# Performance work log

Measured on AMD Instinct MI355X. Metric: run time of the kernel, lower is better.

The kernel has to match this reference:

```python
import jax, jax.numpy as jnp
import numpy as np

N = 200000          # total nodes across the batch of graphs
IN_DIM = 320        # pooling_dim (256) + num_context_attrs (64)
POOL_DIM = 256      # output_dim
HID = 128
NUM_GRAPHS = 2000


def setup_inputs() -> dict:
    key = jax.random.key(0)
    k = jax.random.split(key, 6)
    z = jax.random.normal(k[0], (N, IN_DIM), dtype=jnp.float32)
    batch_index = jnp.sort(jax.random.randint(k[1], (N,), 0, NUM_GRAPHS, dtype=jnp.int64))
    # Kaiming-ish small init to keep softmax well-conditioned
    W1 = jax.random.normal(k[2], (HID, IN_DIM), dtype=jnp.float32) * (1.0 / np.sqrt(IN_DIM))
    b1 = jax.random.normal(k[3], (HID,), dtype=jnp.float32) * 0.01
    W2 = jax.random.normal(k[4], (1, HID), dtype=jnp.float32) * (1.0 / np.sqrt(HID))
    b2 = jax.random.normal(k[5], (1,), dtype=jnp.float32) * 0.01
    return {"z": z, "batch_index": batch_index, "W1": W1, "b1": b1,
            "W2": W2, "b2": b2, "num_graphs": NUM_GRAPHS}


def reference(z, batch_index, W1, b1, W2, b2, num_graphs):
    # attention_net: Linear -> ReLU -> Linear, scores: [N, 1]
    h = jax.nn.relu(z @ W1.T + b1)                  # [N, HID]
    scores = h @ W2.T + b2                          # [N, 1]
    # global (over all nodes) max-subtract + softmax along dim 0
    scores = scores - jnp.max(scores, axis=0, keepdims=True)
    weights = jax.nn.softmax(scores, axis=0)        # [N, 1]
    # weighted scatter-mean over graphs keyed by batch_index
    weighted = weights * z[:, :POOL_DIM]            # [N, POOL_DIM]
    sums = jax.ops.segment_sum(weighted, batch_index, num_segments=num_graphs)  # [G, POOL_DIM]
    counts = jax.ops.segment_sum(jnp.ones((z.shape[0],), dtype=z.dtype),
                                 batch_index, num_segments=num_graphs)          # [G]
    pooled = sums / jnp.maximum(counts, 1.0)[:, None]
    return pooled
```

## Files before the change

### kernel.cpp

```cpp
#include <hip/hip_runtime.h>

#define IN_DIM   320
#define POOL_DIM 256
#define HID      128
#define RPB      128
#define NKC      10

typedef __attribute__((ext_vector_type(8))) short bf16x8;
typedef __attribute__((ext_vector_type(4))) float f32x4;

typedef __attribute__((address_space(1))) const unsigned int guint;
typedef __attribute__((address_space(3))) unsigned int luint;

__device__ __forceinline__ void gl_lds16(const void* g, void* l) {
    __builtin_amdgcn_global_load_lds((guint*)g, (luint*)l, 16, 0, 0);
}

__device__ __forceinline__ unsigned fbits(float f) {
    union { float f; unsigned u; } c; c.f = f; return c.u;
}
__device__ __forceinline__ unsigned pack2(unsigned u0, unsigned u1) {
    return __builtin_amdgcn_perm(u1, u0, 0x07060302u);
}

__device__ __forceinline__ void split8(float4 a, float4 b, bf16x8& hi, bf16x8& lo) {
    float f[8] = { a.x, a.y, a.z, a.w, b.x, b.y, b.z, b.w };
    unsigned hu[8], lu[8];
#pragma unroll
    for (int i = 0; i < 8; ++i) {
        unsigned u = fbits(f[i]);
        hu[i] = u;
        float hif = __builtin_bit_cast(float, u & 0xffff0000u);
        lu[i] = fbits(f[i] - hif);
    }
    int4 hp, lp;
    hp.x = pack2(hu[0], hu[1]); hp.y = pack2(hu[2], hu[3]);
    hp.z = pack2(hu[4], hu[5]); hp.w = pack2(hu[6], hu[7]);
    lp.x = pack2(lu[0], lu[1]); lp.y = pack2(lu[2], lu[3]);
    lp.z = pack2(lu[4], lu[5]); lp.w = pack2(lu[6], lu[7]);
    hi = __builtin_bit_cast(bf16x8, hp);
    lo = __builtin_bit_cast(bf16x8, lp);
}

__global__ __launch_bounds__(256) void pack_w1_kernel(
    const float* __restrict__ W1, ushort* __restrict__ Wpk)
{
    const int i = blockIdx.x * 256 + threadIdx.x;
    if (i >= NKC * 8 * 2 * 64) return;
    const int kc   = i >> 10;
    const int r    = i & 1023;
    const int ht   = r >> 7;
    const int r2   = r & 127;
    const int s    = r2 >> 6;
    const int lane = r2 & 63;
    const int h    = ht * 16 + (lane & 15);
    const int k0   = kc * 32 + (lane >> 4) * 8;

    ushort v[8];
#pragma unroll
    for (int j = 0; j < 8; ++j) {
        const float f = W1[(size_t)h * IN_DIM + k0 + j];
        const unsigned u = fbits(f);
        if (s == 0) {
            v[j] = (ushort)(u >> 16);
        } else {
            const float hif = __builtin_bit_cast(float, u & 0xffff0000u);
            v[j] = (ushort)(fbits(f - hif) >> 16);
        }
    }
    ushort* dst = Wpk + (size_t)i * 8;
#pragma unroll
    for (int j = 0; j < 8; ++j) dst[j] = v[j];
}

__global__ __launch_bounds__(256) void attn_scores_mfma(
    const float* __restrict__ z, const ushort* __restrict__ Wpk,
    const float* __restrict__ b1, const float* __restrict__ W2,
    const float* __restrict__ b2,
    float* __restrict__ scores, float* __restrict__ bmax,
    float* __restrict__ bsum, int N)
{
    __shared__ float4 wbuf[2][1024];
    __shared__ float4 zbuf[2][1024];
    __shared__ float  sblk[RPB];

    const int tid  = threadIdx.x;
    const int wid  = tid >> 6;
    const int lane = tid & 63;
    const int lm   = lane & 15;
    const int lg   = lane >> 4;
    const int r0   = blockIdx.x * RPB;

    const char* zsrc[4];
#pragma unroll
    for (int j = 0; j < 4; ++j) {
        const int s   = tid + j * 256;
        const int row = s >> 3;
        const int q   = (s & 7) ^ (row & 7);
        int gr = r0 + row; if (gr > N - 1) gr = N - 1;
        zsrc[j] = (const char*)z + (size_t)gr * (IN_DIM * 4) + q * 16;
    }

    #define STAGE_W(kc_, b_)                                                  \
        { const char* src = (const char*)Wpk + (size_t)(kc_) * 16384;         \
          char* dst = (char*)&wbuf[b_][0];                                    \
          _Pragma("unroll")                                                   \
          for (int j = 0; j < 4; ++j) {                                       \
              const int o = (tid + j * 256) * 16;                             \
              gl_lds16(src + o, dst + o);                                     \
          } }

    #define STAGE_Z(kc_, b_)                                                  \
        { char* dst = (char*)&zbuf[b_][0];                                    \
          _Pragma("unroll")                                                   \
          for (int j = 0; j < 4; ++j) {                                       \
              const int o = (tid + j * 256) * 16;                             \
              gl_lds16(zsrc[j] + (kc_) * 128, dst + o);                       \
          } }

    f32x4 acc[2][8];
#pragma unroll
    for (int rt = 0; rt < 2; ++rt)
#pragma unroll
        for (int ht = 0; ht < 8; ++ht) acc[rt][ht] = (f32x4){0.f, 0.f, 0.f, 0.f};

    const int lr0 = wid * 32 + lm;
    const int lr1 = lr0 + 16;
    const int i00 = lr0 * 8 + ((2 * lg)     ^ (lr0 & 7));
    const int i01 = lr0 * 8 + ((2 * lg + 1) ^ (lr0 & 7));
    const int i10 = lr1 * 8 + ((2 * lg)     ^ (lr1 & 7));
    const int i11 = lr1 * 8 + ((2 * lg + 1) ^ (lr1 & 7));

    STAGE_Z(0, 0);
    STAGE_W(0, 0);
    __syncthreads();

#pragma unroll
    for (int kc = 0; kc < NKC; ++kc) {
        const int cb  = kc & 1;
        const int nb2 = cb ^ 1;

        if (kc + 1 < NKC) {
            STAGE_Z(kc + 1, nb2);
            STAGE_W(kc + 1, nb2);
        }

        bf16x8 a0h, a0l, a1h, a1l;
        {
            const float4* zb = &zbuf[cb][0];
            const float4 x0 = zb[i00];
            const float4 x1 = zb[i01];
            const float4 y0 = zb[i10];
            const float4 y1 = zb[i11];
            split8(x0, x1, a0h, a0l);
            split8(y0, y1, a1h, a1l);
        }

        const char* wb_base = (const char*)&wbuf[cb][0] + lane * 16;
#pragma unroll
        for (int ht = 0; ht < 8; ++ht) {
            const bf16x8 bh = *(const bf16x8*)(wb_base + ht * 2048);
            const bf16x8 bl = *(const bf16x8*)(wb_base + ht * 2048 + 1024);
            acc[0][ht] = __builtin_amdgcn_mfma_f32_16x16x32_bf16(a0h, bh, acc[0][ht], 0, 0, 0);
            acc[0][ht] = __builtin_amdgcn_mfma_f32_16x16x32_bf16(a0l, bh, acc[0][ht], 0, 0, 0);
            acc[0][ht] = __builtin_amdgcn_mfma_f32_16x16x32_bf16(a0h, bl, acc[0][ht], 0, 0, 0);
            acc[1][ht] = __builtin_amdgcn_mfma_f32_16x16x32_bf16(a1h, bh, acc[1][ht], 0, 0, 0);
            acc[1][ht] = __builtin_amdgcn_mfma_f32_16x16x32_bf16(a1l, bh, acc[1][ht], 0, 0, 0);
            acc[1][ht] = __builtin_amdgcn_mfma_f32_16x16x32_bf16(a1h, bl, acc[1][ht], 0, 0, 0);
        }

        if (kc + 1 < NKC) __syncthreads();
    }

    float b1v[8], w2v[8];
#pragma unroll
    for (int ht = 0; ht < 8; ++ht) {
        b1v[ht] = b1[ht * 16 + lm];
        w2v[ht] = W2[ht * 16 + lm];
    }
    const float b2v = b2[0];

#pragma unroll
    for (int rt = 0; rt < 2; ++rt) {
#pragma unroll
        for (int reg = 0; reg < 4; ++reg) {
            float s = 0.f;
#pragma unroll
            for (int ht = 0; ht < 8; ++ht)
                s += fmaxf(acc[rt][ht][reg] + b1v[ht], 0.f) * w2v[ht];
            s += __shfl_xor(s, 1);
            s += __shfl_xor(s, 2);
            s += __shfl_xor(s, 4);
            s += __shfl_xor(s, 8);
            s += b2v;
            if (lm == 0) {
                const int rloc = wid * 32 + rt * 16 + lg * 4 + reg;
                const int grow = r0 + rloc;
                if (grow < N) {
                    scores[grow] = s;
                    sblk[rloc] = s;
                } else {
                    sblk[rloc] = -1e30f;
                }
            }
        }
    }
    __syncthreads();

    if (tid < 64) {
        const float v0 = sblk[tid];
        const float v1 = sblk[tid + 64];
        float m = fmaxf(v0, v1);
#pragma unroll
        for (int d = 1; d < 64; d <<= 1) m = fmaxf(m, __shfl_xor(m, d, 64));
        float e = __expf(v0 - m) + __expf(v1 - m);
#pragma unroll
        for (int d = 1; d < 64; d <<= 1) e += __shfl_xor(e, d, 64);
        if (tid == 0) {
            bmax[blockIdx.x] = m;
            bsum[blockIdx.x] = e;
        }
    }
}

__global__ __launch_bounds__(256) void softmax_reduce_kernel(
    const float* __restrict__ bmax, const float* __restrict__ bsum,
    float* __restrict__ red, int nb)
{
    __shared__ float sm[4];
    __shared__ float ss[4];
    const int tid = threadIdx.x;

    float m = -1e30f;
    for (int i = tid; i < nb; i += 256) m = fmaxf(m, bmax[i]);
#pragma unroll
    for (int d = 1; d < 64; d <<= 1) m = fmaxf(m, __shfl_xor(m, d, 64));
    if ((tid & 63) == 0) sm[tid >> 6] = m;
    __syncthreads();
    const float gmax = fmaxf(fmaxf(sm[0], sm[1]), fmaxf(sm[2], sm[3]));

    float s = 0.f;
    for (int i = tid; i < nb; i += 256) s += bsum[i] * __expf(bmax[i] - gmax);
#pragma unroll
    for (int d = 1; d < 64; d <<= 1) s += __shfl_xor(s, d, 64);
    if ((tid & 63) == 0) ss[tid >> 6] = s;
    __syncthreads();
    if (tid == 0) {
        red[0] = gmax;
        red[1] = ss[0] + ss[1] + ss[2] + ss[3];
    }
}

__device__ __forceinline__ int lower_bound(const int* __restrict__ a, int n, int key)
{
    int lo = 0, hi = n;
    while (lo < hi) {
        int mid = (lo + hi) >> 1;
        if (a[mid] < key) lo = mid + 1; else hi = mid;
    }
    return lo;
}

__global__ __launch_bounds__(256) void pool_kernel(
    const float* __restrict__ z, const int* __restrict__ bidx,
    const float* __restrict__ scores, const float* __restrict__ red,
    float* __restrict__ out, int N)
{
    const int g    = blockIdx.x;
    const int lane = threadIdx.x & 63;
    const int rg   = threadIdx.x >> 6;
    __shared__ int se[2];
    __shared__ f32x4 pred[4][64];

    if (threadIdx.x == 0) {
        se[0] = lower_bound(bidx, N, g);
        se[1] = lower_bound(bidx, N, g + 1);
    }
    __syncthreads();
    const int start = se[0], end = se[1];
    const float gmax    = red[0];
    const float inv_den = 1.0f / red[1];

    const f32x4* zf = (const f32x4*)z;

    f32x4 acc = (f32x4){0.f, 0.f, 0.f, 0.f};
    for (int i = start + rg; i < end; i += 4) {
        const float w = __expf(scores[i] - gmax);
        acc += w * zf[(size_t)i * 80 + lane];
    }
    pred[rg][lane] = acc;
    __syncthreads();

    if (rg == 0) {
        const f32x4 s = (pred[0][lane] + pred[1][lane]) +
                        (pred[2][lane] + pred[3][lane]);
        const int cnt = end - start;
        const float sc = inv_den / fmaxf((float)cnt, 1.0f);
        ((f32x4*)out)[(size_t)g * 64 + lane] = s * sc;
    }
}

extern "C" void kernel_launch(void* const* d_in, const int* in_sizes, int n_in,
                              void* d_out, int out_size, void* d_ws, size_t ws_size,
                              hipStream_t stream)
{
    const float* z    = (const float*)d_in[0];
    const int*   bidx = (const int*)  d_in[1];
    const float* W1   = (const float*)d_in[2];
    const float* b1   = (const float*)d_in[3];
    const float* W2   = (const float*)d_in[4];
    const float* b2   = (const float*)d_in[5];
    float*       out  = (float*)d_out;

    const int N  = in_sizes[0] / IN_DIM;
    const int G  = out_size / POOL_DIM;
    const int nb = (N + RPB - 1) / RPB;

    float*  scores = (float*)d_ws;
    float*  bmax   = scores + 200000;
    float*  bsum   = bmax + 1600;
    float*  red    = bsum + 1600;
    ushort* Wpk    = (ushort*)(red + 16);

    pack_w1_kernel<<<(NKC * 8 * 2 * 64 + 255) / 256, 256, 0, stream>>>(W1, Wpk);
    attn_scores_mfma<<<nb, 256, 0, stream>>>(z, Wpk, b1, W2, b2,
                                             scores, bmax, bsum, N);
    softmax_reduce_kernel<<<1, 256, 0, stream>>>(bmax, bsum, red, nb);
    pool_kernel<<<G, 256, 0, stream>>>(z, bidx, scores, red, out, N);
}
```

Measured before the change: 116.8 us.

## Fuse segment pooling into score kernel by keeping z tile resident in LDS

The score kernel now keeps the whole z tile (64 rows × 256 pooled columns) resident in LDS and, after computing scores, accumulates per-segment partial weighted sums using the block-local max. A small combine kernel then rescales those partials by the block max relative to the global max. This removes the second full read of z from global memory that the old pool kernel needed. In exchange it halves rows per block, adds a partial-sum buffer with up to 8 segments per block, and assumes 64 consecutive sorted rows span at most 8 graphs and that N is a multiple of 64 (the bidx read is not bounds-checked).

Result: slower. 146.8 us (+25.7%).

```diff
diff --git a/kernel.cpp b/kernel.cpp
--- a/kernel.cpp
+++ b/kernel.cpp
@@ -3,8 +3,10 @@
 #define IN_DIM   320
 #define POOL_DIM 256
 #define HID      128
-#define RPB      128
+#define RPB      64
+#define NT       128
 #define NKC      10
+#define NSEG     8
 
 typedef __attribute__((ext_vector_type(8))) short bf16x8;
 typedef __attribute__((ext_vector_type(4))) float f32x4;
@@ -73,50 +75,61 @@
     for (int j = 0; j < 8; ++j) dst[j] = v[j];
 }
 
-__global__ __launch_bounds__(256) void attn_scores_mfma(
+__global__ __launch_bounds__(NT) void attn_fused(
     const float* __restrict__ z, const ushort* __restrict__ Wpk,
     const float* __restrict__ b1, const float* __restrict__ W2,
-    const float* __restrict__ b2,
-    float* __restrict__ scores, float* __restrict__ bmax,
-    float* __restrict__ bsum, int N)
-{
-    __shared__ float4 wbuf[2][1024];
-    __shared__ float4 zbuf[2][1024];
-    __shared__ float  sblk[RPB];
+    const float* __restrict__ b2, const int* __restrict__ bidx,
+    float* __restrict__ bmax, float* __restrict__ bsum,
+    float* __restrict__ P, int* __restrict__ meta, int N)
+{
+    __shared__ f32x4 zkeep4[8 * 512];
+    __shared__ f32x4 wbuf4[1024];
+    float* sblk    = (float*)wbuf4;
+    int*   seg_s0  = (int*)((char*)wbuf4 + 256);
+    int*   seg_gid = (int*)((char*)wbuf4 + 528);
+    float* shm_m   = (float*)((char*)wbuf4 + 784);
+    int*   shm_ns  = (int*)((char*)wbuf4 + 788);
 
     const int tid  = threadIdx.x;
     const int wid  = tid >> 6;
     const int lane = tid & 63;
     const int lm   = lane & 15;
     const int lg   = lane >> 4;
-    const int r0   = blockIdx.x * RPB;
+    const int bk   = blockIdx.x;
+    const int r0   = bk * RPB;
 
     const char* zsrc[4];
 #pragma unroll
     for (int j = 0; j < 4; ++j) {
-        const int s   = tid + j * 256;
+        const int s   = j * NT + tid;
         const int row = s >> 3;
         const int q   = (s & 7) ^ (row & 7);
         int gr = r0 + row; if (gr > N - 1) gr = N - 1;
         zsrc[j] = (const char*)z + (size_t)gr * (IN_DIM * 4) + q * 16;
     }
 
-    #define STAGE_W(kc_, b_)                                                  \
-        { const char* src = (const char*)Wpk + (size_t)(kc_) * 16384;         \
-          char* dst = (char*)&wbuf[b_][0];                                    \
+    #define STAGE_ZC(kc_, sl_)                                                \
+        { char* dst = (char*)zkeep4 + (sl_) * 8192;                           \
           _Pragma("unroll")                                                   \
           for (int j = 0; j < 4; ++j) {                                       \
-              const int o = (tid + j * 256) * 16;                             \
+              const int o = (j * NT + tid) * 16;                              \
+              gl_lds16(zsrc[j] + (kc_) * 128, dst + o);                       \
+          } }
+
+    #define STAGE_W(kc_)                                                      \
+        { const char* src = (const char*)Wpk + (size_t)(kc_) * 16384;         \
+          char* dst = (char*)wbuf4;                                           \
+          _Pragma("unroll")                                                   \
+          for (int j = 0; j < 8; ++j) {                                       \
+              const int o = (j * NT + tid) * 16;                              \
               gl_lds16(src + o, dst + o);                                     \
           } }
 
-    #define STAGE_Z(kc_, b_)                                                  \
-        { char* dst = (char*)&zbuf[b_][0];                                    \
-          _Pragma("unroll")                                                   \
-          for (int j = 0; j < 4; ++j) {                                       \
-              const int o = (tid + j * 256) * 16;                             \
-              gl_lds16(zsrc[j] + (kc_) * 128, dst + o);                       \
-          } }
+    STAGE_ZC(8, 6);
+    STAGE_W(8);
+    STAGE_ZC(9, 7);
+    STAGE_ZC(0, 0); STAGE_ZC(1, 1); STAGE_ZC(2, 2);
+    STAGE_ZC(3, 3); STAGE_ZC(4, 4); STAGE_ZC(5, 5);
 
     f32x4 acc[2][8];
 #pragma unroll
@@ -126,50 +139,49 @@
 
     const int lr0 = wid * 32 + lm;
     const int lr1 = lr0 + 16;
-    const int i00 = lr0 * 8 + ((2 * lg)     ^ (lr0 & 7));
-    const int i01 = lr0 * 8 + ((2 * lg + 1) ^ (lr0 & 7));
-    const int i10 = lr1 * 8 + ((2 * lg)     ^ (lr1 & 7));
-    const int i11 = lr1 * 8 + ((2 * lg + 1) ^ (lr1 & 7));
-
-    STAGE_Z(0, 0);
-    STAGE_W(0, 0);
-    __syncthreads();
-
-#pragma unroll
-    for (int kc = 0; kc < NKC; ++kc) {
-        const int cb  = kc & 1;
-        const int nb2 = cb ^ 1;
-
-        if (kc + 1 < NKC) {
-            STAGE_Z(kc + 1, nb2);
-            STAGE_W(kc + 1, nb2);
-        }
+    const int j00 = lr0 * 8 + ((2 * lg)     ^ (lr0 & 7));
+    const int j01 = lr0 * 8 + ((2 * lg + 1) ^ (lr0 & 7));
+    const int j10 = lr1 * 8 + ((2 * lg)     ^ (lr1 & 7));
+    const int j11 = lr1 * 8 + ((2 * lg + 1) ^ (lr1 & 7));
+
+    const int ord_kc[NKC] = {8, 9, 0, 1, 2, 3, 4, 5, 6, 7};
+    const int ord_sl[NKC] = {6, 7, 0, 1, 2, 3, 4, 5, 6, 7};
+
+#pragma unroll
+    for (int t = 0; t < NKC; ++t) {
+        __syncthreads();
+
+        const char* wb_base = (const char*)wbuf4 + lane * 16;
+        bf16x8 bh[8], bl[8];
+#pragma unroll
+        for (int ht = 0; ht < 8; ++ht) {
+            bh[ht] = *(const bf16x8*)(wb_base + ht * 2048);
+            bl[ht] = *(const bf16x8*)(wb_base + ht * 2048 + 1024);
+        }
+        const float4* zb = (const float4*)&zkeep4[ord_sl[t] * 512];
+        const float4 x0 = zb[j00];
+        const float4 x1 = zb[j01];
+        const float4 y0 = zb[j10];
+        const float4 y1 = zb[j11];
+
+        __syncthreads();
+
+        if (t + 1 < NKC) STAGE_W(ord_kc[t + 1]);
+        if (t == 0) STAGE_ZC(6, 6);
+        if (t == 1) STAGE_ZC(7, 7);
 
         bf16x8 a0h, a0l, a1h, a1l;
-        {
-            const float4* zb = &zbuf[cb][0];
-            const float4 x0 = zb[i00];
-            const float4 x1 = zb[i01];
-            const float4 y0 = zb[i10];
-            const float4 y1 = zb[i11];
-            split8(x0, x1, a0h, a0l);
-            split8(y0, y1, a1h, a1l);
-        }
-
-        const char* wb_base = (const char*)&wbuf[cb][0] + lane * 16;
+        split8(x0, x1, a0h, a0l);
+        split8(y0, y1, a1h, a1l);
 #pragma unroll
         for (int ht = 0; ht < 8; ++ht) {
-            const bf16x8 bh = *(const bf16x8*)(wb_base + ht * 2048);
-            const bf16x8 bl = *(const bf16x8*)(wb_base + ht * 2048 + 1024);
-            acc[0][ht] = __builtin_amdgcn_mfma_f32_16x16x32_bf16(a0h, bh, acc[0][ht], 0, 0, 0);
-            acc[0][ht] = __builtin_amdgcn_mfma_f32_16x16x32_bf16(a0l, bh, acc[0][ht], 0, 0, 0);
-            acc[0][ht] = __builtin_amdgcn_mfma_f32_16x16x32_bf16(a0h, bl, acc[0][ht], 0, 0, 0);
-            acc[1][ht] = __builtin_amdgcn_mfma_f32_16x16x32_bf16(a1h, bh, acc[1][ht], 0, 0, 0);
-            acc[1][ht] = __builtin_amdgcn_mfma_f32_16x16x32_bf16(a1l, bh, acc[1][ht], 0, 0, 0);
-            acc[1][ht] = __builtin_amdgcn_mfma_f32_16x16x32_bf16(a1h, bl, acc[1][ht], 0, 0, 0);
-        }
-
-        if (kc + 1 < NKC) __syncthreads();
+            acc[0][ht] = __builtin_amdgcn_mfma_f32_16x16x32_bf16(a0h, bh[ht], acc[0][ht], 0, 0, 0);
+            acc[0][ht] = __builtin_amdgcn_mfma_f32_16x16x32_bf16(a0l, bh[ht], acc[0][ht], 0, 0, 0);
+            acc[0][ht] = __builtin_amdgcn_mfma_f32_16x16x32_bf16(a0h, bl[ht], acc[0][ht], 0, 0, 0);
+            acc[1][ht] = __builtin_amdgcn_mfma_f32_16x16x32_bf16(a1h, bh[ht], acc[1][ht], 0, 0, 0);
+            acc[1][ht] = __builtin_amdgcn_mfma_f32_16x16x32_bf16(a1l, bh[ht], acc[1][ht], 0, 0, 0);
+            acc[1][ht] = __builtin_amdgcn_mfma_f32_16x16x32_bf16(a1h, bl[ht], acc[1][ht], 0, 0, 0);
+        }
     }
 
     float b1v[8], w2v[8];
@@ -195,32 +207,58 @@
             s += b2v;
             if (lm == 0) {
                 const int rloc = wid * 32 + rt * 16 + lg * 4 + reg;
-                const int grow = r0 + rloc;
-                if (grow < N) {
-                    scores[grow] = s;
-                    sblk[rloc] = s;
-                } else {
-                    sblk[rloc] = -1e30f;
-                }
+                sblk[rloc] = s;
             }
         }
     }
     __syncthreads();
 
     if (tid < 64) {
-        const float v0 = sblk[tid];
-        const float v1 = sblk[tid + 64];
-        float m = fmaxf(v0, v1);
+        const float v = sblk[tid];
+        float m = v;
 #pragma unroll
         for (int d = 1; d < 64; d <<= 1) m = fmaxf(m, __shfl_xor(m, d, 64));
-        float e = __expf(v0 - m) + __expf(v1 - m);
-#pragma unroll
-        for (int d = 1; d < 64; d <<= 1) e += __shfl_xor(e, d, 64);
+        float e = __expf(v - m);
+        float es = e;
+#pragma unroll
+        for (int d = 1; d < 64; d <<= 1) es += __shfl_xor(es, d, 64);
+
+        const int g    = bidx[r0 + tid];
+        const int prev = __shfl_up(g, 1);
+        const int flag = (tid == 0) || (g != prev);
+        const unsigned long long mask = __ballot(flag);
+        const int idx = (int)__popcll(mask & ((1ull << tid) - 1ull));
+        const int ns  = (int)__popcll(mask);
+        if (flag) { seg_s0[idx] = tid; seg_gid[idx] = g; }
         if (tid == 0) {
-            bmax[blockIdx.x] = m;
-            bsum[blockIdx.x] = e;
-        }
-    }
+            bmax[bk] = m; bsum[bk] = es;
+            shm_m[0] = m; shm_ns[0] = ns;
+            seg_s0[ns] = RPB;
+        }
+    }
+    __syncthreads();
+
+    const float mb   = shm_m[0];
+    const int   nseg = shm_ns[0];
+    const int   rg   = wid;
+    const int   kcp  = lane >> 3;
+    const int   qp   = lane & 7;
+    f32x4* P4 = (f32x4*)P;
+
+#pragma unroll
+    for (int s = 0; s < NSEG; ++s) {
+        if (s >= nseg) break;
+        const int rs = seg_s0[s];
+        const int re = seg_s0[s + 1];
+        f32x4 a = (f32x4){0.f, 0.f, 0.f, 0.f};
+        for (int row = rs + rg; row < re; row += 2) {
+            const float w = __expf(sblk[row] - mb);
+            a += w * zkeep4[kcp * 512 + row * 8 + (qp ^ (row & 7))];
+        }
+        P4[(((size_t)bk * NSEG + s) * 2 + rg) * 64 + lane] = a;
+    }
+    if (tid < NSEG)
+        meta[bk * NSEG + tid] = (tid < nseg) ? seg_gid[tid] : -1;
 }
 
 __global__ __launch_bounds__(256) void softmax_reduce_kernel(
@@ -261,43 +299,38 @@
     return lo;
 }
 
-__global__ __launch_bounds__(256) void pool_kernel(
-    const float* __restrict__ z, const int* __restrict__ bidx,
-    const float* __restrict__ scores, const float* __restrict__ red,
-    float* __restrict__ out, int N)
+__global__ __launch_bounds__(64) void combine_kernel(
+    const int* __restrict__ bidx, const float* __restrict__ bmax,
+    const float* __restrict__ red, const float* __restrict__ P,
+    const int* __restrict__ meta, float* __restrict__ out, int N)
 {
     const int g    = blockIdx.x;
-    const int lane = threadIdx.x & 63;
-    const int rg   = threadIdx.x >> 6;
-    __shared__ int se[2];
-    __shared__ f32x4 pred[4][64];
-
-    if (threadIdx.x == 0) {
-        se[0] = lower_bound(bidx, N, g);
-        se[1] = lower_bound(bidx, N, g + 1);
-    }
-    __syncthreads();
-    const int start = se[0], end = se[1];
+    const int lane = threadIdx.x;
+
+    const int start = lower_bound(bidx, N, g);
+    const int end   = lower_bound(bidx, N, g + 1);
     const float gmax    = red[0];
     const float inv_den = 1.0f / red[1];
 
-    const f32x4* zf = (const f32x4*)z;
-
-    f32x4 acc = (f32x4){0.f, 0.f, 0.f, 0.f};
-    for (int i = start + rg; i < end; i += 4) {
-        const float w = __expf(scores[i] - gmax);
-        acc += w * zf[(size_t)i * 80 + lane];
-    }
-    pred[rg][lane] = acc;
-    __syncthreads();
-
-    if (rg == 0) {
-        const f32x4 s = (pred[0][lane] + pred[1][lane]) +
-                        (pred[2][lane] + pred[3][lane]);
-        const int cnt = end - start;
-        const float sc = inv_den / fmaxf((float)cnt, 1.0f);
-        ((f32x4*)out)[(size_t)g * 64 + lane] = s * sc;
-    }
+    f32x4 a = (f32x4){0.f, 0.f, 0.f, 0.f};
+    if (end > start) {
+        const int b0 = start >> 6;
+        const int b1 = (end - 1) >> 6;
+        const f32x4* P4 = (const f32x4*)P;
+        for (int b = b0; b <= b1; ++b) {
+            int s = -1;
+#pragma unroll
+            for (int k = 0; k < NSEG; ++k)
+                if (meta[b * NSEG + k] == g) s = k;
+            if (s < 0) continue;
+            const size_t base = (((size_t)b * NSEG + s) * 2) * 64 + lane;
+            const f32x4 t2 = P4[base] + P4[base + 64];
+            a += __expf(bmax[b] - gmax) * t2;
+        }
+    }
+    const int cnt = end - start;
+    const float sc = inv_den / fmaxf((float)cnt, 1.0f);
+    ((f32x4*)out)[(size_t)g * 64 + lane] = a * sc;
 }
 
 extern "C" void kernel_launch(void* const* d_in, const int* in_sizes, int n_in,
@@ -316,15 +349,16 @@
     const int G  = out_size / POOL_DIM;
     const int nb = (N + RPB - 1) / RPB;
 
-    float*  scores = (float*)d_ws;
-    float*  bmax   = scores + 200000;
-    float*  bsum   = bmax + 1600;
-    float*  red    = bsum + 1600;
-    ushort* Wpk    = (ushort*)(red + 16);
+    float*  bmax = (float*)d_ws;
+    float*  bsum = bmax + 3200;
+    float*  red  = bsum + 3200;
+    int*    meta = (int*)(red + 16);
+    float*  P    = (float*)(meta + 3200 * NSEG);
+    ushort* Wpk  = (ushort*)(P + (size_t)3200 * NSEG * 2 * 256);
 
     pack_w1_kernel<<<(NKC * 8 * 2 * 64 + 255) / 256, 256, 0, stream>>>(W1, Wpk);
-    attn_scores_mfma<<<nb, 256, 0, stream>>>(z, Wpk, b1, W2, b2,
-                                             scores, bmax, bsum, N);
+    attn_fused<<<nb, NT, 0, stream>>>(z, Wpk, b1, W2, b2, bidx,
+                                      bmax, bsum, P, meta, N);
     softmax_reduce_kernel<<<1, 256, 0, stream>>>(bmax, bsum, red, nb);
-    pool_kernel<<<G, 256, 0, stream>>>(z, bidx, scores, red, out, N);
-}
+    combine_kernel<<<G, 64, 0, stream>>>(bidx, bmax, red, P, meta, out, N);
+}
```
